# Kernel tuning notes

Hardware: AMD Instinct MI355X
Metric: run time of the kernel (lower is better)

The kernel has to match this reference:

```python
import jax, jax.numpy as jnp
import numpy as np

B, S, D = 4, 2048, 1024
E, H = 1024, 16
HD = E // H
TEMPERATURE = 1.0


def setup_inputs() -> dict:
    key = jax.random.key(0)
    ks = jax.random.split(key, 6)
    x = jax.random.normal(ks[0], (B, S, D), dtype=jnp.float32)
    src_key_padding_mask = jnp.zeros((B, S), dtype=bool)  # unused by module
    matrix_mask = jax.random.normal(ks[1], (B, S, S), dtype=jnp.float32)
    # Xavier-uniform linear weights (torch Linear stores [out, in])
    lim_qkv = float(np.sqrt(6.0 / (D + 3 * E)))
    qkv_w = jax.random.uniform(ks[2], (3 * E, D), dtype=jnp.float32, minval=-lim_qkv, maxval=lim_qkv)
    qkv_b = jnp.zeros((3 * E,), dtype=jnp.float32)
    lim_o = float(np.sqrt(6.0 / (E + E)))
    o_w = jax.random.uniform(ks[3], (E, E), dtype=jnp.float32, minval=-lim_o, maxval=lim_o)
    o_b = jnp.zeros((E,), dtype=jnp.float32)
    return {"x": x, "src_key_padding_mask": src_key_padding_mask, "matrix_mask": matrix_mask,
            "qkv_w": qkv_w, "qkv_b": qkv_b, "o_w": o_w, "o_b": o_b}


def reference(x, src_key_padding_mask, matrix_mask, qkv_w, qkv_b, o_w, o_b):
    b, s, _ = x.shape
    qkv = x @ qkv_w.T + qkv_b                      # [B,S,3E]
    qkv = qkv.reshape(b, s, H, 3 * HD).transpose(0, 2, 1, 3)  # [B,H,S,3*HD]
    q, k, v = jnp.split(qkv, 3, axis=-1)           # each [B,H,S,HD]
    scale = 1.0 / np.sqrt(HD)
    logits = jnp.einsum('bhqd,bhkd->bhqk', q, k) * scale + matrix_mask[:, None, :, :]
    attn = jax.nn.softmax(logits / TEMPERATURE, axis=-1)  # [B,H,S,S]
    # dropout=0.0, eval mode -> no-op
    values = jnp.einsum('bhqk,bhkd->bhqd', attn, v)       # [B,H,S,HD]
    values = values.transpose(0, 2, 1, 3).reshape(b, s, E)
    o = values @ o_w.T + o_b                       # [B,S,E]
    attention_mean = jnp.mean(attn, axis=1)        # [B,S,S]
    return (o, attention_mean)
```

## Files before the change

### kernel.cpp

```cpp
#include <hip/hip_runtime.h>

#define B_ 4
#define S_ 2048
#define D_ 1024
#define E_ 1024
#define H_ 16
#define HD_ 64
#define SCALE 0.125f
#define LOG2E 1.44269504f
#define C1_ (SCALE * LOG2E)

typedef __bf16 bf16;
typedef __bf16 bf16x8 __attribute__((ext_vector_type(8)));
typedef __bf16 bf16x4 __attribute__((ext_vector_type(4)));
typedef float f32x4 __attribute__((ext_vector_type(4)));
typedef _Float16 f16x8 __attribute__((ext_vector_type(8)));
typedef _Float16 f16x4 __attribute__((ext_vector_type(4)));

static __device__ __forceinline__ f32x4 mfma16(bf16x8 a, bf16x8 b, f32x4 c) {
  return __builtin_amdgcn_mfma_f32_16x16x32_bf16(a, b, c, 0, 0, 0);
}

typedef __attribute__((address_space(3))) void lvoid;
typedef const __attribute__((address_space(1))) void gvoid;
static __device__ __forceinline__ void gload16(const void* g, void* l) {
  __builtin_amdgcn_global_load_lds((gvoid*)g, (lvoid*)l, 16, 0, 0);
}

static __device__ __forceinline__ float exp2a(float x) {
  float r;
  asm("v_exp_f32 %0, %1" : "=v"(r) : "v"(x));
  return r;
}

static __device__ __forceinline__ int rsw(int row) {
  return (row & 3) | (((row >> 3) & 1) << 2);
}

__global__ __launch_bounds__(256) void k_cvtall(const float* __restrict__ x, bf16* __restrict__ xb,
                                                const float* __restrict__ qkvw, bf16* __restrict__ wb,
                                                const float* __restrict__ ow, bf16* __restrict__ owb,
                                                const float* __restrict__ msk, _Float16* __restrict__ bm) {
  int bid = blockIdx.x;
  int i;
  if (bid < 8192) {
    i = bid * 256 + threadIdx.x;
    float4 v = reinterpret_cast<const float4*>(x)[i];
    bf16x4 o = { (bf16)v.x, (bf16)v.y, (bf16)v.z, (bf16)v.w };
    reinterpret_cast<bf16x4*>(xb)[i] = o;
  } else if (bid < 11264) {
    i = (bid - 8192) * 256 + threadIdx.x;
    float4 v = reinterpret_cast<const float4*>(qkvw)[i];
    bf16x4 o = { (bf16)v.x, (bf16)v.y, (bf16)v.z, (bf16)v.w };
    reinterpret_cast<bf16x4*>(wb)[i] = o;
  } else if (bid < 12288) {
    i = (bid - 11264) * 256 + threadIdx.x;
    float4 v = reinterpret_cast<const float4*>(ow)[i];
    bf16x4 o = { (bf16)v.x, (bf16)v.y, (bf16)v.z, (bf16)v.w };
    reinterpret_cast<bf16x4*>(owb)[i] = o;
  } else {
    i = (bid - 12288) * 256 + threadIdx.x;
    float4 v = reinterpret_cast<const float4*>(msk)[i];
    f16x4 o = { (_Float16)(v.x * LOG2E), (_Float16)(v.y * LOG2E),
                (_Float16)(v.z * LOG2E), (_Float16)(v.w * LOG2E) };
    reinterpret_cast<f16x4*>(bm)[i] = o;
  }
}

__global__ __launch_bounds__(256) void k_qkv(const bf16* __restrict__ xb,
                                             const bf16* __restrict__ wb,
                                             const float* __restrict__ qkvb,
                                             bf16* __restrict__ Qw,
                                             bf16* __restrict__ Kw,
                                             bf16* __restrict__ Vtw) {
  __shared__ __align__(16) bf16 lA[128 * 32];
  __shared__ __align__(16) bf16 lB[128 * 32];
  const int tid = threadIdx.x, lane = tid & 63, wv = tid >> 6;
  const int u = lane >> 4, c = lane & 15;
  const int wr = wv >> 1, wc = wv & 1;
  const int m0 = blockIdx.y * 128;
  const int n0 = blockIdx.x * 128;
  const int sr = tid >> 2, sk = (tid & 3) * 8;
  const bf16* gA = xb + (size_t)(m0 + sr) * D_ + sk;
  const bf16* gB = wb + (size_t)(n0 + sr) * D_ + sk;
  bf16* lpA = lA + wv * 512;
  bf16* lpB = lB + wv * 512;
  f32x4 acc[4][4] = {};
  for (int k0 = 0; k0 < D_; k0 += 32) {
    gload16(gA + k0, lpA);
    gload16(gA + 64 * D_ + k0, lpA + 2048);
    gload16(gB + k0, lpB);
    gload16(gB + 64 * D_ + k0, lpB + 2048);
    __syncthreads();
    bf16x8 af[4], bfr[4];
#pragma unroll
    for (int m = 0; m < 4; ++m)
      af[m] = *(const bf16x8*)(lA + (wr * 64 + m * 16 + c) * 32 + u * 8);
#pragma unroll
    for (int n = 0; n < 4; ++n)
      bfr[n] = *(const bf16x8*)(lB + (wc * 64 + n * 16 + c) * 32 + u * 8);
#pragma unroll
    for (int m = 0; m < 4; ++m)
#pragma unroll
      for (int n = 0; n < 4; ++n)
        acc[m][n] = mfma16(af[m], bfr[n], acc[m][n]);
    __syncthreads();
  }
#pragma unroll
  for (int n = 0; n < 4; ++n) {
    int nn = n0 + wc * 64 + n * 16 + c;
    float bias = qkvb[nn];
    int h = nn / 192;
    int rem = nn - h * 192;
#pragma unroll
    for (int m = 0; m < 4; ++m) {
#pragma unroll
      for (int r = 0; r < 4; ++r) {
        int q = m0 + wr * 64 + m * 16 + 4 * u + r;
        int bb = q >> 11, s = q & 2047;
        bf16 v = (bf16)(acc[m][n][r] + bias);
        if (rem < 64)       Qw[((bb * H_ + h) * S_ + s) * HD_ + rem] = v;
        else if (rem < 128) Kw[((bb * H_ + h) * S_ + s) * HD_ + (rem - 64)] = v;
        else                Vtw[((bb * H_ + h) * HD_ + (rem - 128)) * S_ + s] = v;
      }
    }
  }
}

#define PV_TILE2(HC, HN, BS, KT, PF)                                          \
  {                                                                           \
    f32x4 sA[4], sB[4];                                                       \
    _Pragma("unroll")                                                         \
    for (int f = 0; f < 4; ++f) {                                             \
      int rk = 32 * (f & 1) + 8 * (c >> 2) + 4 * (f >> 1) + (c & 3);          \
      int sw = rsw(rk);                                                       \
      bf16x8 k0 = *(const bf16x8*)&kl[BS][rk * 64 + ((u ^ sw) * 8)];          \
      bf16x8 k1 = *(const bf16x8*)&kl[BS][rk * 64 + (((4 + u) ^ sw) * 8)];    \
      f32x4 a = {};                                                           \
      a = mfma16(k0, aqA0, a);                                                \
      a = mfma16(k1, aqA1, a);                                                \
      sA[f] = a;                                                              \
      f32x4 bb2 = {};                                                         \
      bb2 = mfma16(k0, aqB0, bb2);                                            \
      bb2 = mfma16(k1, aqB1, bb2);                                            \
      sB[f] = bb2;                                                            \
    }                                                                         \
    if (PF) {                                                                 \
      const bf16* ksrc = Kb + (size_t)((KT) + 1) * 64 * HD_;                  \
      gload16(ksrc + ksw1, (bf16*)kl[(BS) ^ 1] + wv * 512);                   \
      gload16(ksrc + ksw2, (bf16*)kl[(BS) ^ 1] + 2048 + wv * 512);            \
      const bf16* vsrc = Vb + (size_t)((KT) + 1) * 64;                        \
      gload16(vsrc + vsw1, (bf16*)vl[(BS) ^ 1] + wv * 512);                   \
      gload16(vsrc + vsw2, (bf16*)vl[(BS) ^ 1] + 2048 + wv * 512);            \
      const _Float16* nA = bmrA + ((KT) + 1) * 64 + 8 * u;                    \
      const _Float16* nB = bmrB + ((KT) + 1) * 64 + 8 * u;                    \
      HN[0] = *(const f16x8*)(nA);                                            \
      HN[1] = *(const f16x8*)(nA + 32);                                       \
      HN[2] = *(const f16x8*)(nB);                                            \
      HN[3] = *(const f16x8*)(nB + 32);                                       \
    }                                                                         \
    float pA[16], pB[16];                                                     \
    _Pragma("unroll")                                                         \
    for (int f = 0; f < 4; ++f) {                                             \
      _Pragma("unroll")                                                       \
      for (int j = 0; j < 4; ++j) {                                           \
        float p = exp2a(sA[f][j] * C1_ + (float)HC[f & 1][4 * (f >> 1) + j]); \
        lsumA += p;                                                           \
        pA[f * 4 + j] = p;                                                    \
        float q2 = exp2a(sB[f][j] * C1_ +                                     \
                         (float)HC[2 + (f & 1)][4 * (f >> 1) + j]);           \
        lsumB += q2;                                                          \
        pB[f * 4 + j] = q2;                                                   \
      }                                                                       \
    }                                                                         \
    bf16x8 bpA0 = { (bf16)pA[0],  (bf16)pA[1],  (bf16)pA[2],  (bf16)pA[3],    \
                    (bf16)pA[8],  (bf16)pA[9],  (bf16)pA[10], (bf16)pA[11] }; \
    bf16x8 bpA1 = { (bf16)pA[4],  (bf16)pA[5],  (bf16)pA[6],  (bf16)pA[7],    \
                    (bf16)pA[12], (bf16)pA[13], (bf16)pA[14], (bf16)pA[15] }; \
    bf16x8 bpB0 = { (bf16)pB[0],  (bf16)pB[1],  (bf16)pB[2],  (bf16)pB[3],    \
                    (bf16)pB[8],  (bf16)pB[9],  (bf16)pB[10], (bf16)pB[11] }; \
    bf16x8 bpB1 = { (bf16)pB[4],  (bf16)pB[5],  (bf16)pB[6],  (bf16)pB[7],    \
                    (bf16)pB[12], (bf16)pB[13], (bf16)pB[14], (bf16)pB[15] }; \
    __builtin_amdgcn_s_setprio(1);                                            \
    _Pragma("unroll")                                                         \
    for (int g = 0; g < 4; ++g) {                                             \
      int rv = g * 16 + c;                                                    \
      int swv = rsw(rv);                                                      \
      bf16x8 v0 = *(const bf16x8*)&vl[BS][rv * 64 + ((u ^ swv) * 8)];         \
      bf16x8 v1 = *(const bf16x8*)&vl[BS][rv * 64 + (((4 + u) ^ swv) * 8)];   \
      accA[g] = mfma16(v0, bpA0, accA[g]);                                    \
      accA[g] = mfma16(v1, bpA1, accA[g]);                                    \
      accB[g] = mfma16(v0, bpB0, accB[g]);                                    \
      accB[g] = mfma16(v1, bpB1, accB[g]);                                    \
    }                                                                         \
    __builtin_amdgcn_s_setprio(0);                                            \
    asm volatile("s_waitcnt vmcnt(4) lgkmcnt(0)" ::: "memory");               \
    __builtin_amdgcn_s_barrier();                                             \
  }

__global__ __launch_bounds__(256) void k_pv(const bf16* __restrict__ Qw,
                                            const bf16* __restrict__ Kw,
                                            const bf16* __restrict__ Vtw,
                                            const _Float16* __restrict__ bmask,
                                            float* __restrict__ li_ws,
                                            bf16* __restrict__ valw) {
  __shared__ __align__(16) bf16 kl[2][64 * 64];
  __shared__ __align__(16) bf16 vl[2][64 * 64];
  const int tid = threadIdx.x, lane = tid & 63, wv = tid >> 6;
  const int u = lane >> 4, c = lane & 15;
  const int qt = blockIdx.x, h = blockIdx.y, b = blockIdx.z;
  const bf16* Qb = Qw + (size_t)(b * H_ + h) * S_ * HD_;
  const bf16* Kb = Kw + (size_t)(b * H_ + h) * S_ * HD_;
  const bf16* Vb = Vtw + (size_t)(b * H_ + h) * HD_ * S_;
  const int qrA = qt * 128 + wv * 32 + c;
  const int qrB = qrA + 16;
  bf16x8 aqA0 = *(const bf16x8*)(Qb + (size_t)qrA * HD_ + u * 8);
  bf16x8 aqA1 = *(const bf16x8*)(Qb + (size_t)qrA * HD_ + 32 + u * 8);
  bf16x8 aqB0 = *(const bf16x8*)(Qb + (size_t)qrB * HD_ + u * 8);
  bf16x8 aqB1 = *(const bf16x8*)(Qb + (size_t)qrB * HD_ + 32 + u * 8);
  const _Float16* bmrA = bmask + (size_t)b * S_ * S_ + (size_t)qrA * S_;
  const _Float16* bmrB = bmask + (size_t)b * S_ * S_ + (size_t)qrB * S_;
  const int r1 = tid >> 3, s1 = (tid & 7) ^ rsw(tid >> 3);
  const int g2i = tid + 256;
  const int r2 = g2i >> 3, s2 = (g2i & 7) ^ rsw(g2i >> 3);
  const int ksw1 = (r1 * 8 + s1) * 8, ksw2 = (r2 * 8 + s2) * 8;
  const int vsw1 = r1 * S_ + s1 * 8, vsw2 = r2 * S_ + s2 * 8;
  gload16(Kb + ksw1, (bf16*)kl[0] + wv * 512);
  gload16(Kb + ksw2, (bf16*)kl[0] + 2048 + wv * 512);
  gload16(Vb + vsw1, (bf16*)vl[0] + wv * 512);
  gload16(Vb + vsw2, (bf16*)vl[0] + 2048 + wv * 512);
  f16x8 hmA[4], hmB[4];
  hmA[0] = *(const f16x8*)(bmrA + 8 * u);
  hmA[1] = *(const f16x8*)(bmrA + 32 + 8 * u);
  hmA[2] = *(const f16x8*)(bmrB + 8 * u);
  hmA[3] = *(const f16x8*)(bmrB + 32 + 8 * u);
  f32x4 accA[4] = {}, accB[4] = {};
  float lsumA = 0.f, lsumB = 0.f;
  __syncthreads();
  for (int kt2 = 0; kt2 < 16; ++kt2) {
    PV_TILE2(hmA, hmB, 0, 2 * kt2, true);
    PV_TILE2(hmB, hmA, 1, 2 * kt2 + 1, (kt2 < 15));
  }
  lsumA += __shfl_xor(lsumA, 16, 64);
  lsumA += __shfl_xor(lsumA, 32, 64);
  lsumB += __shfl_xor(lsumB, 16, 64);
  lsumB += __shfl_xor(lsumB, 32, 64);
  float liA = 1.f / lsumA, liB = 1.f / lsumB;
  if (u == 0) {
    li_ws[(b * H_ + h) * S_ + qrA] = liA;
    li_ws[(b * H_ + h) * S_ + qrB] = liB;
  }
#pragma unroll
  for (int g = 0; g < 4; ++g) {
    bf16x4 pkA = { (bf16)(accA[g][0] * liA), (bf16)(accA[g][1] * liA),
                   (bf16)(accA[g][2] * liA), (bf16)(accA[g][3] * liA) };
    *(bf16x4*)(&valw[(size_t)(b * S_ + qrA) * E_ + h * HD_ + g * 16 + 4 * u]) = pkA;
    bf16x4 pkB = { (bf16)(accB[g][0] * liB), (bf16)(accB[g][1] * liB),
                   (bf16)(accB[g][2] * liB), (bf16)(accB[g][3] * liB) };
    *(bf16x4*)(&valw[(size_t)(b * S_ + qrB) * E_ + h * HD_ + g * 16 + 4 * u]) = pkB;
  }
}

#define MEAN_PHASE(QC0, QC1, QC2, QC3, QN0, QN1, QN2, QN3, BS, HH, PF)         \
  {                                                                            \
    if (PF) {                                                                  \
      const bf16* ksrc = Kw + (size_t)(bh0 + (HH) + 1) * S_ * HD_ +            \
                         (size_t)kt * 64 * HD_;                                \
      gload16(ksrc + sw1, (bf16*)kl2[(BS) ^ 1] + wv * 512);                    \
      gload16(ksrc + sw2, (bf16*)kl2[(BS) ^ 1] + 2048 + wv * 512);             \
      __builtin_amdgcn_sched_barrier(0);                                       \
    }                                                                          \
    bf16x8 kf[8];                                                              \
    _Pragma("unroll")                                                          \
    for (int f = 0; f < 4; ++f) {                                              \
      int row = f * 16 + c;                                                    \
      int sw = row & 7;                                                        \
      kf[2 * f]     = *(const bf16x8*)&kl2[BS][row * 64 + ((u ^ sw) * 8)];     \
      kf[2 * f + 1] = *(const bf16x8*)&kl2[BS][row * 64 + (((4 + u) ^ sw) * 8)];\
    }                                                                          \
    if (PF) {                                                                  \
      const bf16* Qn = Qw + (size_t)(bh0 + (HH) + 1) * S_ * HD_ +              \
                       (size_t)(qrow0 + c) * HD_ + u * 8;                      \
      QN0 = *(const bf16x8*)(Qn);                                              \
      QN1 = *(const bf16x8*)(Qn + 32);                                         \
      QN2 = *(const bf16x8*)(Qn + 64 * HD_);                                   \
      QN3 = *(const bf16x8*)(Qn + 64 * HD_ + 32);                              \
    }                                                                          \
    float llA = li_l[(HH) * 128 + wv * 16 + c];                                \
    float llB = li_l[(HH) * 128 + 64 + wv * 16 + c];                           \
    _Pragma("unroll")                                                          \
    for (int f = 0; f < 4; ++f) {                                              \
      f32x4 a = {};                                                            \
      a = mfma16(kf[2 * f], QC0, a);                                           \
      a = mfma16(kf[2 * f + 1], QC1, a);                                       \
      f32x4 bb = {};                                                           \
      bb = mfma16(kf[2 * f], QC2, bb);                                         \
      bb = mfma16(kf[2 * f + 1], QC3, bb);                                     \
      _Pragma("unroll")                                                        \
      for (int j = 0; j < 4; ++j) {                                            \
        maccA[f][j] += exp2a(a[j] * C1_ + (float)mhA[f][j]) * llA;             \
        maccB[f][j] += exp2a(bb[j] * C1_ + (float)mhB[f][j]) * llB;            \
      }                                                                        \
    }                                                                          \
    asm volatile("s_waitcnt vmcnt(4) lgkmcnt(0)" ::: "memory");                \
    __builtin_amdgcn_s_barrier();                                              \
  }

__global__ __launch_bounds__(256) void k_mean(const bf16* __restrict__ Qw,
                                              const bf16* __restrict__ Kw,
                                              const _Float16* __restrict__ bmask,
                                              const float* __restrict__ li_ws,
                                              float* __restrict__ mean_out) {
  __shared__ float li_l[H_ * 128];
  __shared__ __align__(16) bf16 kl2[2][64 * 64];
  const int tid = threadIdx.x, lane = tid & 63, wv = tid >> 6;
  const int u = lane >> 4, c = lane & 15;
  const int qt = blockIdx.x, kt = blockIdx.y, b = blockIdx.z;
  const int bh0 = b * H_;
  for (int i = tid; i < H_ * 128; i += 256) {
    int hh = i >> 7, q = i & 127;
    li_l[i] = li_ws[(bh0 + hh) * S_ + qt * 128 + q];
  }
  const int qrow0 = qt * 128 + wv * 16;
  f16x4 mhA[4], mhB[4];
  {
    const _Float16* bmpA = bmask + (size_t)b * S_ * S_ +
                           (size_t)(qrow0 + c) * S_ + (size_t)kt * 64 + 4 * u;
    const _Float16* bmpB = bmpA + (size_t)64 * S_;
#pragma unroll
    for (int f = 0; f < 4; ++f) {
      mhA[f] = *(const f16x4*)(bmpA + f * 16);
      mhB[f] = *(const f16x4*)(bmpB + f * 16);
    }
  }
  const int gg1 = wv * 64 + lane;
  const int gg2 = gg1 + 256;
  const int sw1 = (gg1 ^ ((gg1 >> 3) & 7)) * 8;
  const int sw2 = (gg2 ^ ((gg2 >> 3) & 7)) * 8;
  {
    const bf16* K0 = Kw + (size_t)bh0 * S_ * HD_ + (size_t)kt * 64 * HD_;
    gload16(K0 + sw1, (bf16*)kl2[0] + wv * 512);
    gload16(K0 + sw2, (bf16*)kl2[0] + 2048 + wv * 512);
  }
  bf16x8 qA0, qA1, qA2, qA3, qB0, qB1, qB2, qB3;
  {
    const bf16* Q0 = Qw + (size_t)bh0 * S_ * HD_ + (size_t)(qrow0 + c) * HD_ + u * 8;
    qA0 = *(const bf16x8*)Q0;
    qA1 = *(const bf16x8*)(Q0 + 32);
    qA2 = *(const bf16x8*)(Q0 + 64 * HD_);
    qA3 = *(const bf16x8*)(Q0 + 64 * HD_ + 32);
  }
  f32x4 maccA[4] = {}, maccB[4] = {};
  __syncthreads();
  for (int h2 = 0; h2 < 8; ++h2) {
    MEAN_PHASE(qA0, qA1, qA2, qA3, qB0, qB1, qB2, qB3, 0, 2 * h2, true);
    MEAN_PHASE(qB0, qB1, qB2, qB3, qA0, qA1, qA2, qA3, 1, 2 * h2 + 1, (h2 < 7));
  }
#pragma unroll
  for (int f = 0; f < 4; ++f) {
    f32x4 moA = maccA[f] * (1.f / 16.f);
    *(f32x4*)&mean_out[(size_t)b * S_ * S_ + (size_t)(qrow0 + c) * S_ +
                       (size_t)kt * 64 + f * 16 + 4 * u] = moA;
    f32x4 moB = maccB[f] * (1.f / 16.f);
    *(f32x4*)&mean_out[(size_t)b * S_ * S_ + (size_t)(qrow0 + 64 + c) * S_ +
                       (size_t)kt * 64 + f * 16 + 4 * u] = moB;
  }
}

__global__ __launch_bounds__(256) void k_oproj(const bf16* __restrict__ vb,
                                               const bf16* __restrict__ wo,
                                               const float* __restrict__ ob,
                                               float* __restrict__ out) {
  __shared__ __align__(16) bf16 lA[128 * 32];
  __shared__ __align__(16) bf16 lB[128 * 32];
  const int tid = threadIdx.x, lane = tid & 63, wv = tid >> 6;
  const int u = lane >> 4, c = lane & 15;
  const int wr = wv >> 1, wc = wv & 1;
  const int m0 = blockIdx.y * 128;
  const int n0 = blockIdx.x * 128;
  const int sr = tid >> 2, sk = (tid & 3) * 8;
  const bf16* gA = vb + (size_t)(m0 + sr) * E_ + sk;
  const bf16* gB = wo + (size_t)(n0 + sr) * E_ + sk;
  bf16* lpA = lA + wv * 512;
  bf16* lpB = lB + wv * 512;
  f32x4 acc[4][4] = {};
  for (int k0 = 0; k0 < E_; k0 += 32) {
    gload16(gA + k0, lpA);
    gload16(gA + 64 * E_ + k0, lpA + 2048);
    gload16(gB + k0, lpB);
    gload16(gB + 64 * E_ + k0, lpB + 2048);
    __syncthreads();
    bf16x8 af[4], bfr[4];
#pragma unroll
    for (int m = 0; m < 4; ++m)
      af[m] = *(const bf16x8*)(lA + (wr * 64 + m * 16 + c) * 32 + u * 8);
#pragma unroll
    for (int n = 0; n < 4; ++n)
      bfr[n] = *(const bf16x8*)(lB + (wc * 64 + n * 16 + c) * 32 + u * 8);
#pragma unroll
    for (int m = 0; m < 4; ++m)
#pragma unroll
      for (int n = 0; n < 4; ++n)
        acc[m][n] = mfma16(af[m], bfr[n], acc[m][n]);
    __syncthreads();
  }
#pragma unroll
  for (int n = 0; n < 4; ++n) {
    int nn = n0 + wc * 64 + n * 16 + c;
    float bias = ob[nn];
#pragma unroll
    for (int m = 0; m < 4; ++m) {
#pragma unroll
      for (int r = 0; r < 4; ++r) {
        int q = m0 + wr * 64 + m * 16 + 4 * u + r;
        out[(size_t)q * E_ + nn] = acc[m][n][r] + bias;
      }
    }
  }
}

extern "C" void kernel_launch(void* const* d_in, const int* in_sizes, int n_in,
                              void* d_out, int out_size, void* d_ws, size_t ws_size,
                              hipStream_t stream) {
  const float* x    = (const float*)d_in[0];
  const float* mmsk = (const float*)d_in[2];
  const float* qkvw = (const float*)d_in[3];
  const float* qkvb = (const float*)d_in[4];
  const float* ow   = (const float*)d_in[5];
  const float* ob   = (const float*)d_in[6];

  char* ws = (char*)d_ws;
  bf16* xb  = (bf16*)(ws);
  bf16* wb  = (bf16*)(ws + (16u << 20));
  bf16* owb = (bf16*)(ws + (22u << 20));
  bf16* Qw  = (bf16*)(ws + (24u << 20));
  bf16* Kw  = (bf16*)(ws + (40u << 20));
  bf16* Vtw = (bf16*)(ws + (56u << 20));
  float* li_ws = (float*)(ws + (16u << 20));
  bf16* values = xb;
  _Float16* bmask = (_Float16*)(ws + (72u << 20));

  float* out_o    = (float*)d_out;
  float* out_mean = out_o + (size_t)B_ * S_ * E_;

  k_cvtall<<<dim3(28672), 256, 0, stream>>>(x, xb, qkvw, wb, ow, owb, mmsk, bmask);
  k_qkv<<<dim3(24, 64), 256, 0, stream>>>(xb, wb, qkvb, Qw, Kw, Vtw);
  k_pv<<<dim3(16, 16, 4), 256, 0, stream>>>(Qw, Kw, Vtw, bmask, li_ws, values);
  k_mean<<<dim3(16, 32, 4), 256, 0, stream>>>(Qw, Kw, bmask, li_ws, out_mean);
  k_oproj<<<dim3(8, 64), 256, 0, stream>>>(values, owb, ob, out_o);
}
```

Measured before the change: 333.7 us.

## Overlap mask and out-proj weight conversion with QKV GEMM blocks

Splits the conversion kernel so that only x and the QKV weight are converted before the QKV projection. The mask conversion (to fp16 scaled by log2e) and the output-projection weight conversion become extra blocks appended to the QKV GEMM grid, so these memory-bound blocks can run alongside the compute-bound GEMM tiles. The grid is flattened to 1D, with GEMM tile indices derived from the block id. Separately, the PV macro's partial vmcnt(4) wait plus raw barrier is replaced by a full __syncthreads, which may drain outstanding prefetch loads and reduce overlap in the attention loop.

New measurement: 331.7 us. About the same (-0.6%).

```diff
diff --git a/kernel.cpp b/kernel.cpp
--- a/kernel.cpp
+++ b/kernel.cpp
@@ -37,10 +37,8 @@
   return (row & 3) | (((row >> 3) & 1) << 2);
 }
 
-__global__ __launch_bounds__(256) void k_cvtall(const float* __restrict__ x, bf16* __restrict__ xb,
-                                                const float* __restrict__ qkvw, bf16* __restrict__ wb,
-                                                const float* __restrict__ ow, bf16* __restrict__ owb,
-                                                const float* __restrict__ msk, _Float16* __restrict__ bm) {
+__global__ __launch_bounds__(256) void k_cvt1(const float* __restrict__ x, bf16* __restrict__ xb,
+                                              const float* __restrict__ qkvw, bf16* __restrict__ wb) {
   int bid = blockIdx.x;
   int i;
   if (bid < 8192) {
@@ -48,38 +46,47 @@
     float4 v = reinterpret_cast<const float4*>(x)[i];
     bf16x4 o = { (bf16)v.x, (bf16)v.y, (bf16)v.z, (bf16)v.w };
     reinterpret_cast<bf16x4*>(xb)[i] = o;
-  } else if (bid < 11264) {
+  } else {
     i = (bid - 8192) * 256 + threadIdx.x;
     float4 v = reinterpret_cast<const float4*>(qkvw)[i];
     bf16x4 o = { (bf16)v.x, (bf16)v.y, (bf16)v.z, (bf16)v.w };
     reinterpret_cast<bf16x4*>(wb)[i] = o;
-  } else if (bid < 12288) {
-    i = (bid - 11264) * 256 + threadIdx.x;
-    float4 v = reinterpret_cast<const float4*>(ow)[i];
-    bf16x4 o = { (bf16)v.x, (bf16)v.y, (bf16)v.z, (bf16)v.w };
-    reinterpret_cast<bf16x4*>(owb)[i] = o;
-  } else {
-    i = (bid - 12288) * 256 + threadIdx.x;
-    float4 v = reinterpret_cast<const float4*>(msk)[i];
-    f16x4 o = { (_Float16)(v.x * LOG2E), (_Float16)(v.y * LOG2E),
-                (_Float16)(v.z * LOG2E), (_Float16)(v.w * LOG2E) };
-    reinterpret_cast<f16x4*>(bm)[i] = o;
-  }
-}
-
-__global__ __launch_bounds__(256) void k_qkv(const bf16* __restrict__ xb,
-                                             const bf16* __restrict__ wb,
-                                             const float* __restrict__ qkvb,
-                                             bf16* __restrict__ Qw,
-                                             bf16* __restrict__ Kw,
-                                             bf16* __restrict__ Vtw) {
+  }
+}
+
+__global__ __launch_bounds__(256) void k_qkvf(const bf16* __restrict__ xb,
+                                              const bf16* __restrict__ wb,
+                                              const float* __restrict__ qkvb,
+                                              bf16* __restrict__ Qw,
+                                              bf16* __restrict__ Kw,
+                                              bf16* __restrict__ Vtw,
+                                              const float* __restrict__ msk,
+                                              _Float16* __restrict__ bm,
+                                              const float* __restrict__ ow,
+                                              bf16* __restrict__ owb) {
   __shared__ __align__(16) bf16 lA[128 * 32];
   __shared__ __align__(16) bf16 lB[128 * 32];
+  const int bid = blockIdx.x;
+  if (bid >= 1536) {
+    if (bid < 17920) {
+      int i = (bid - 1536) * 256 + threadIdx.x;
+      float4 v = reinterpret_cast<const float4*>(msk)[i];
+      f16x4 o = { (_Float16)(v.x * LOG2E), (_Float16)(v.y * LOG2E),
+                  (_Float16)(v.z * LOG2E), (_Float16)(v.w * LOG2E) };
+      reinterpret_cast<f16x4*>(bm)[i] = o;
+    } else {
+      int i = (bid - 17920) * 256 + threadIdx.x;
+      float4 v = reinterpret_cast<const float4*>(ow)[i];
+      bf16x4 o = { (bf16)v.x, (bf16)v.y, (bf16)v.z, (bf16)v.w };
+      reinterpret_cast<bf16x4*>(owb)[i] = o;
+    }
+    return;
+  }
   const int tid = threadIdx.x, lane = tid & 63, wv = tid >> 6;
   const int u = lane >> 4, c = lane & 15;
   const int wr = wv >> 1, wc = wv & 1;
-  const int m0 = blockIdx.y * 128;
-  const int n0 = blockIdx.x * 128;
+  const int n0 = (bid % 24) * 128;
+  const int m0 = (bid / 24) * 128;
   const int sr = tid >> 2, sk = (tid & 3) * 8;
   const bf16* gA = xb + (size_t)(m0 + sr) * D_ + sk;
   const bf16* gB = wb + (size_t)(n0 + sr) * D_ + sk;
@@ -194,8 +201,7 @@
       accB[g] = mfma16(v1, bpB1, accB[g]);                                    \
     }                                                                         \
     __builtin_amdgcn_s_setprio(0);                                            \
-    asm volatile("s_waitcnt vmcnt(4) lgkmcnt(0)" ::: "memory");               \
-    __builtin_amdgcn_s_barrier();                                             \
+    __syncthreads();                                                          \
   }
 
 __global__ __launch_bounds__(256) void k_pv(const bf16* __restrict__ Qw,
@@ -443,8 +449,9 @@
   float* out_o    = (float*)d_out;
   float* out_mean = out_o + (size_t)B_ * S_ * E_;
 
-  k_cvtall<<<dim3(28672), 256, 0, stream>>>(x, xb, qkvw, wb, ow, owb, mmsk, bmask);
-  k_qkv<<<dim3(24, 64), 256, 0, stream>>>(xb, wb, qkvb, Qw, Kw, Vtw);
+  k_cvt1<<<dim3(11264), 256, 0, stream>>>(x, xb, qkvw, wb);
+  k_qkvf<<<dim3(18944), 256, 0, stream>>>(xb, wb, qkvb, Qw, Kw, Vtw,
+                                          mmsk, bmask, ow, owb);
   k_pv<<<dim3(16, 16, 4), 256, 0, stream>>>(Qw, Kw, Vtw, bmask, li_ws, values);
   k_mean<<<dim3(16, 32, 4), 256, 0, stream>>>(Qw, Kw, bmask, li_ws, out_mean);
   k_oproj<<<dim3(8, 64), 256, 0, stream>>>(values, owb, ob, out_o);
```
